# Performance work log

Measured on AMD Instinct MI355X. Metric: run time of the kernel, lower is better.

## Reference

```python
import jax, jax.numpy as jnp
import numpy as np
from jax import lax

N = 128   # batch
H = 1024  # hidden size h
D = 1024  # output size d


def setup_inputs() -> dict:
    key = jax.random.key(0)
    k = jax.random.split(key, 7)
    s_ih = 1.0 / np.sqrt(H)
    inp = {
        "hT": jax.random.normal(k[0], (N, H), dtype=jnp.float32),
        # LSTMCell params (PyTorch layout: [4h, h], gate order i,f,g,o)
        "W_ih": jax.random.uniform(k[1], (4 * H, H), dtype=jnp.float32, minval=-s_ih, maxval=s_ih),
        "W_hh": jax.random.uniform(k[2], (4 * H, H), dtype=jnp.float32, minval=-s_ih, maxval=s_ih),
        "b_ih": jax.random.uniform(k[3], (4 * H,), dtype=jnp.float32, minval=-s_ih, maxval=s_ih),
        "b_hh": jax.random.uniform(k[4], (4 * H,), dtype=jnp.float32, minval=-s_ih, maxval=s_ih),
        # fc1: Linear(h, d)
        "W_fc": jax.random.uniform(k[5], (D, H), dtype=jnp.float32, minval=-s_ih, maxval=s_ih),
        "b_fc": jax.random.uniform(k[6], (D,), dtype=jnp.float32, minval=-s_ih, maxval=s_ih),
        "t": 256,
    }
    return inp


def reference(hT, W_ih, W_hh, b_ih, b_hh, W_fc, b_fc, t):
    n, h = hT.shape

    def step(carry, _):
        x, hx, cx = carry  # x: LSTM input this step; at step 0 it is hT, else prev h
        gates = x @ W_ih.T + b_ih + hx @ W_hh.T + b_hh  # [n, 4h]
        i, f, g, o = jnp.split(gates, 4, axis=-1)
        i = jax.nn.sigmoid(i)
        f = jax.nn.sigmoid(f)
        g = jnp.tanh(g)
        o = jax.nn.sigmoid(o)
        c_new = f * cx + i * g
        h_new = o * jnp.tanh(c_new)
        # next input is the hidden state just produced (all_hs[-1])
        return (h_new, h_new, c_new), h_new

    zeros = jnp.zeros_like(hT)
    _, hs = lax.scan(step, (hT, zeros, zeros), None, length=t)  # [t, n, h]
    recons = hs @ W_fc.T + b_fc  # [t, n, d]
    return jnp.transpose(recons, (1, 0, 2))  # [n, t, d]
```

## Files before the change

### kernel.cpp

```cpp
#include <hip/hip_runtime.h>

#define Hh 1024
#define NBATCH 128
#define TSTEPS 256
#define DOUT 1024
#define SLOT (NBATCH * Hh)

typedef _Float16 half8 __attribute__((ext_vector_type(8)));
typedef float floatx4 __attribute__((ext_vector_type(4)));

__device__ __forceinline__ float fast_sigmoid(float x) {
  float e = __expf(-x);
  return __builtin_amdgcn_rcpf(1.0f + e);
}
__device__ __forceinline__ float fast_tanh(float x) {
  x = fminf(15.0f, fmaxf(-15.0f, x));
  float e = __expf(-2.0f * x);
  return 1.0f - 2.0f * e * __builtin_amdgcn_rcpf(1.0f + e);
}

__global__ void prep_kernel(const float* __restrict__ W_ih, const float* __restrict__ W_hh,
                            const float* __restrict__ W_fc, const float* __restrict__ b_ih,
                            const float* __restrict__ b_hh, const float* __restrict__ hT,
                            _Float16* __restrict__ w_ih_h, _Float16* __restrict__ w_sum_h,
                            _Float16* __restrict__ w_fc_h, float* __restrict__ b_sum,
                            _Float16* __restrict__ hs0, unsigned* __restrict__ flags) {
  int i0 = blockIdx.x * blockDim.x + threadIdx.x;
  int stride = gridDim.x * blockDim.x;
  for (int i = i0; i < 4096 * 1024; i += stride) {
    float a = W_ih[i];
    w_ih_h[i] = (_Float16)a;
    w_sum_h[i] = (_Float16)(a + W_hh[i]);
  }
  for (int i = i0; i < 1024 * 1024; i += stride) w_fc_h[i] = (_Float16)W_fc[i];
  for (int i = i0; i < 4096; i += stride) b_sum[i] = b_ih[i] + b_hh[i];
  for (int i = i0; i < NBATCH * Hh; i += stride) hs0[i] = (_Float16)hT[i];
  for (int i = i0; i < 512; i += stride) flags[i] = 0;
}

__global__ __launch_bounds__(512, 2) void lstm_kernel(
    const _Float16* __restrict__ w_ih_h, const _Float16* __restrict__ w_sum_h,
    const float* __restrict__ b_sum, _Float16* __restrict__ hs,
    unsigned* __restrict__ flags, const _Float16* __restrict__ w_fc,
    const float* __restrict__ b_fc, float* __restrict__ out) {
  unsigned* xcd_ctr = flags + 256;
  const int tid = threadIdx.x;
  const int wave = tid >> 6;
  const int lane = tid & 63;
  const int l15 = lane & 15;
  const int quad = lane >> 4;

  __shared__ unsigned role_sh;
  {
    unsigned xcd;
    asm volatile("s_getreg_b32 %0, hwreg(HW_REG_XCC_ID)" : "=s"(xcd));
    if (tid == 0) role_sh = (xcd << 8) | atomicAdd(&xcd_ctr[xcd], 1u);
  }
  __syncthreads();
  const int g = role_sh >> 8;
  const int jb = role_sh & 255;
  const int n0 = g * 16;
  const int j0 = jb * 32;
  const int kbase = wave * 128;
  const int oc = wave & 1;
  const int rp = (wave >> 1) & 1;
  const int rr = (wave >> 2) & 1;
  unsigned* gflags = flags + g * 32;
  unsigned* pollp = gflags + wave * 4 + (lane & 3);

  __shared__ float2 part[8][2][4][2][64];
  __shared__ floatx4 fcpart[8][2][64];

  float bias[4];
#pragma unroll
  for (int gt = 0; gt < 4; ++gt) bias[gt] = b_sum[gt * 1024 + j0 + oc * 16 + l15];

  const int fc_col = tid & 31;
  const int fc_row = tid >> 5;
  const float bfc = b_fc[j0 + fc_col];
  const int fc_half = fc_col >> 4;
  const int fc_lsrc = (fc_row >> 2) * 16 + (fc_col & 15);
  const int fc_comp = fc_row & 3;

  half8 B[4][2][4];
  half8 Bfc[2][4];
  float cst = 0.0f;

  auto load_B = [&](const _Float16* w) {
#pragma unroll
    for (int gt = 0; gt < 4; ++gt)
#pragma unroll
      for (int ct = 0; ct < 2; ++ct) {
        const _Float16* p =
            w + (size_t)(gt * 1024 + j0 + ct * 16 + l15) * Hh + kbase + quad * 8;
#pragma unroll
        for (int ks = 0; ks < 4; ++ks) B[gt][ct][ks] = *(const half8*)(p + ks * 32);
      }
  };
  {
#pragma unroll
    for (int ct = 0; ct < 2; ++ct) {
      const _Float16* p = w_fc + (size_t)(j0 + ct * 16 + l15) * Hh + kbase + quad * 8;
#pragma unroll
      for (int ks = 0; ks < 4; ++ks) Bfc[ct][ks] = *(const half8*)(p + ks * 32);
    }
  }

  auto poll = [&](int tgt) {
    while (1) {
      unsigned v = __hip_atomic_load(pollp, __ATOMIC_RELAXED, __HIP_MEMORY_SCOPE_AGENT);
      if (__all((int)(v >= (unsigned)tgt))) break;
    }
  };

  auto do_step = [&](const _Float16* hsrc, _Float16* hdst, int s) {
    poll(s);
    floatx4 acc[2][4] = {};
    floatx4 f0 = {}, f1 = {};
    const _Float16* ap = hsrc + (size_t)(n0 + l15) * Hh + kbase + quad * 8;
#pragma unroll
    for (int ks = 0; ks < 4; ++ks) {
      half8 a = *(const half8*)(ap + ks * 32);
#pragma unroll
      for (int ct = 0; ct < 2; ++ct)
#pragma unroll
        for (int gt = 0; gt < 4; ++gt)
          acc[ct][gt] =
              __builtin_amdgcn_mfma_f32_16x16x32_f16(a, B[gt][ct][ks], acc[ct][gt], 0, 0, 0);
      if (s >= 1) {
        f0 = __builtin_amdgcn_mfma_f32_16x16x32_f16(a, Bfc[0][ks], f0, 0, 0, 0);
        f1 = __builtin_amdgcn_mfma_f32_16x16x32_f16(a, Bfc[1][ks], f1, 0, 0, 0);
      }
    }
#pragma unroll
    for (int ct = 0; ct < 2; ++ct)
#pragma unroll
      for (int gt = 0; gt < 4; ++gt) {
        float2 lo, hi;
        lo.x = acc[ct][gt][0]; lo.y = acc[ct][gt][1];
        hi.x = acc[ct][gt][2]; hi.y = acc[ct][gt][3];
        part[wave][ct][gt][0][lane] = lo;
        part[wave][ct][gt][1][lane] = hi;
      }
    if (s >= 1) {
      fcpart[wave][0][lane] = f0;
      fcpart[wave][1][lane] = f1;
    }
    __syncthreads();

    float gv[4];
#pragma unroll
    for (int gt = 0; gt < 4; ++gt) {
      float s2 = bias[gt];
#pragma unroll
      for (int src = 0; src < 8; ++src) {
        float2 p = part[src][oc][gt][rp][lane];
        s2 += rr ? p.y : p.x;
      }
      gv[gt] = s2;
    }
    {
      float ig = fast_sigmoid(gv[0]);
      float fg = fast_sigmoid(gv[1]);
      float gg = fast_tanh(gv[2]);
      float og = fast_sigmoid(gv[3]);
      float c = fg * cst + ig * gg;
      cst = c;
      float h = og * fast_tanh(c);
      int row = n0 + quad * 4 + rp * 2 + rr;
      _Float16 hv = (_Float16)h;
      unsigned short ub;
      __builtin_memcpy(&ub, &hv, 2);
      __hip_atomic_store((unsigned short*)(hdst + (size_t)row * Hh + j0 + oc * 16 + l15),
                         ub, __ATOMIC_RELAXED, __HIP_MEMORY_SCOPE_AGENT);
    }
    if (s >= 1) {
      float fsum = bfc;
#pragma unroll
      for (int src = 0; src < 8; ++src) fsum += fcpart[src][fc_half][fc_lsrc][fc_comp];
      out[((size_t)(n0 + fc_row) * TSTEPS + (s - 1)) * DOUT + j0 + fc_col] = fsum;
    }
    __syncthreads();
    if (tid == 0) {
      __hip_atomic_store(&gflags[jb], (unsigned)(s + 1), __ATOMIC_RELAXED,
                         __HIP_MEMORY_SCOPE_AGENT);
    }
  };

  load_B(w_ih_h);
  do_step(hs, hs + SLOT, 0);
  load_B(w_sum_h);
  for (int s = 1; s < TSTEPS; ++s)
    do_step(hs + (size_t)s * SLOT, hs + (size_t)(s + 1) * SLOT, s);

  {
    unsigned* ep = gflags + (lane & 31);
    while (1) {
      unsigned v = __hip_atomic_load(ep, __ATOMIC_RELAXED, __HIP_MEMORY_SCOPE_AGENT);
      if (__all((int)(v >= (unsigned)TSTEPS))) break;
    }
    asm volatile("" ::: "memory");
    floatx4 f0 = {}, f1 = {};
    const _Float16* ap =
        hs + (size_t)TSTEPS * SLOT + (size_t)(n0 + l15) * Hh + kbase + quad * 8;
#pragma unroll
    for (int ks = 0; ks < 4; ++ks) {
      half8 a = *(const half8*)(ap + ks * 32);
      f0 = __builtin_amdgcn_mfma_f32_16x16x32_f16(a, Bfc[0][ks], f0, 0, 0, 0);
      f1 = __builtin_amdgcn_mfma_f32_16x16x32_f16(a, Bfc[1][ks], f1, 0, 0, 0);
    }
    fcpart[wave][0][lane] = f0;
    fcpart[wave][1][lane] = f1;
    __syncthreads();
    float fsum = bfc;
#pragma unroll
    for (int src = 0; src < 8; ++src) fsum += fcpart[src][fc_half][fc_lsrc][fc_comp];
    out[((size_t)(n0 + fc_row) * TSTEPS + (TSTEPS - 1)) * DOUT + j0 + fc_col] = fsum;
  }
}

extern "C" void kernel_launch(void* const* d_in, const int* in_sizes, int n_in,
                              void* d_out, int out_size, void* d_ws, size_t ws_size,
                              hipStream_t stream) {
  const float* hT   = (const float*)d_in[0];
  const float* W_ih = (const float*)d_in[1];
  const float* W_hh = (const float*)d_in[2];
  const float* b_ih = (const float*)d_in[3];
  const float* b_hh = (const float*)d_in[4];
  const float* W_fc = (const float*)d_in[5];
  const float* b_fc = (const float*)d_in[6];
  float* out = (float*)d_out;

  char* ws = (char*)d_ws;
  unsigned* flags   = (unsigned*)ws;
  float* b_sum      = (float*)(ws + 4096);
  _Float16* w_ih_h  = (_Float16*)(ws + 65536);
  _Float16* w_sum_h = w_ih_h + (size_t)4096 * 1024;
  _Float16* w_fc_h  = w_sum_h + (size_t)4096 * 1024;
  _Float16* hs      = w_fc_h + (size_t)1024 * 1024;

  prep_kernel<<<4096, 256, 0, stream>>>(W_ih, W_hh, W_fc, b_ih, b_hh, hT,
                                        w_ih_h, w_sum_h, w_fc_h, b_sum, hs, flags);
  lstm_kernel<<<256, 512, 0, stream>>>(w_ih_h, w_sum_h, b_sum, hs, flags,
                                       w_fc_h, b_fc, out);
}
```

Baseline: 984.9 us.

## Fuse weight conversion into LSTM kernel and drop separate prep kernel

Removes the prep kernel that converted W_ih, W_ih+W_hh, W_fc and hT to fp16 in workspace. Each persistent block now loads its fp32 weight slices directly, sums and converts them in registers, reads hT straight for step 0, and sums the biases itself. The flags are cleared with a hipMemsetAsync. This avoids a full pass writing and re-reading about 18 MB of fp16 weights and one kernel launch, at the cost of fp32 loads at startup inside the persistent kernel.

```diff
diff --git a/kernel.cpp b/kernel.cpp
--- a/kernel.cpp
+++ b/kernel.cpp
@@ -19,30 +19,18 @@
   return 1.0f - 2.0f * e * __builtin_amdgcn_rcpf(1.0f + e);
 }
 
-__global__ void prep_kernel(const float* __restrict__ W_ih, const float* __restrict__ W_hh,
-                            const float* __restrict__ W_fc, const float* __restrict__ b_ih,
-                            const float* __restrict__ b_hh, const float* __restrict__ hT,
-                            _Float16* __restrict__ w_ih_h, _Float16* __restrict__ w_sum_h,
-                            _Float16* __restrict__ w_fc_h, float* __restrict__ b_sum,
-                            _Float16* __restrict__ hs0, unsigned* __restrict__ flags) {
-  int i0 = blockIdx.x * blockDim.x + threadIdx.x;
-  int stride = gridDim.x * blockDim.x;
-  for (int i = i0; i < 4096 * 1024; i += stride) {
-    float a = W_ih[i];
-    w_ih_h[i] = (_Float16)a;
-    w_sum_h[i] = (_Float16)(a + W_hh[i]);
-  }
-  for (int i = i0; i < 1024 * 1024; i += stride) w_fc_h[i] = (_Float16)W_fc[i];
-  for (int i = i0; i < 4096; i += stride) b_sum[i] = b_ih[i] + b_hh[i];
-  for (int i = i0; i < NBATCH * Hh; i += stride) hs0[i] = (_Float16)hT[i];
-  for (int i = i0; i < 512; i += stride) flags[i] = 0;
+__device__ __forceinline__ half8 cvt8(float4 x, float4 y) {
+  half8 h = {(_Float16)x.x, (_Float16)x.y, (_Float16)x.z, (_Float16)x.w,
+             (_Float16)y.x, (_Float16)y.y, (_Float16)y.z, (_Float16)y.w};
+  return h;
 }
 
 __global__ __launch_bounds__(512, 2) void lstm_kernel(
-    const _Float16* __restrict__ w_ih_h, const _Float16* __restrict__ w_sum_h,
-    const float* __restrict__ b_sum, _Float16* __restrict__ hs,
-    unsigned* __restrict__ flags, const _Float16* __restrict__ w_fc,
-    const float* __restrict__ b_fc, float* __restrict__ out) {
+    const float* __restrict__ W_ih, const float* __restrict__ W_hh,
+    const float* __restrict__ b_ih, const float* __restrict__ b_hh,
+    const float* __restrict__ hT, const float* __restrict__ W_fc,
+    const float* __restrict__ b_fc, _Float16* __restrict__ hs,
+    unsigned* __restrict__ flags, float* __restrict__ out) {
   unsigned* xcd_ctr = flags + 256;
   const int tid = threadIdx.x;
   const int wave = tid >> 6;
@@ -73,7 +61,10 @@
 
   float bias[4];
 #pragma unroll
-  for (int gt = 0; gt < 4; ++gt) bias[gt] = b_sum[gt * 1024 + j0 + oc * 16 + l15];
+  for (int gt = 0; gt < 4; ++gt) {
+    int idx = gt * 1024 + j0 + oc * 16 + l15;
+    bias[gt] = b_ih[idx] + b_hh[idx];
+  }
 
   const int fc_col = tid & 31;
   const int fc_row = tid >> 5;
@@ -86,23 +77,52 @@
   half8 Bfc[2][4];
   float cst = 0.0f;
 
-  auto load_B = [&](const _Float16* w) {
+  auto load_B_ih = [&]() {
 #pragma unroll
     for (int gt = 0; gt < 4; ++gt)
 #pragma unroll
       for (int ct = 0; ct < 2; ++ct) {
-        const _Float16* p =
-            w + (size_t)(gt * 1024 + j0 + ct * 16 + l15) * Hh + kbase + quad * 8;
-#pragma unroll
-        for (int ks = 0; ks < 4; ++ks) B[gt][ct][ks] = *(const half8*)(p + ks * 32);
+        const float* p =
+            W_ih + (size_t)(gt * 1024 + j0 + ct * 16 + l15) * Hh + kbase + quad * 8;
+#pragma unroll
+        for (int ks = 0; ks < 4; ++ks) {
+          float4 x = *(const float4*)(p + ks * 32);
+          float4 y = *(const float4*)(p + ks * 32 + 4);
+          B[gt][ct][ks] = cvt8(x, y);
+        }
+      }
+  };
+  auto load_B_sum = [&]() {
+#pragma unroll
+    for (int gt = 0; gt < 4; ++gt)
+#pragma unroll
+      for (int ct = 0; ct < 2; ++ct) {
+        size_t off = (size_t)(gt * 1024 + j0 + ct * 16 + l15) * Hh + kbase + quad * 8;
+        const float* p1 = W_ih + off;
+        const float* p2 = W_hh + off;
+#pragma unroll
+        for (int ks = 0; ks < 4; ++ks) {
+          float4 x1 = *(const float4*)(p1 + ks * 32);
+          float4 y1 = *(const float4*)(p1 + ks * 32 + 4);
+          float4 x2 = *(const float4*)(p2 + ks * 32);
+          float4 y2 = *(const float4*)(p2 + ks * 32 + 4);
+          float4 xs = {x1.x + x2.x, x1.y + x2.y, x1.z + x2.z, x1.w + x2.w};
+          float4 ys = {y1.x + y2.x, y1.y + y2.y, y1.z + y2.z, y1.w + y2.w};
+          B[gt][ct][ks] = cvt8(xs, ys);
+        }
       }
   };
   {
 #pragma unroll
     for (int ct = 0; ct < 2; ++ct) {
-      const _Float16* p = w_fc + (size_t)(j0 + ct * 16 + l15) * Hh + kbase + quad * 8;
-#pragma unroll
-      for (int ks = 0; ks < 4; ++ks) Bfc[ct][ks] = *(const half8*)(p + ks * 32);
+      const float* p =
+          W_fc + (size_t)(j0 + ct * 16 + l15) * Hh + kbase + quad * 8;
+#pragma unroll
+      for (int ks = 0; ks < 4; ++ks) {
+        float4 x = *(const float4*)(p + ks * 32);
+        float4 y = *(const float4*)(p + ks * 32 + 4);
+        Bfc[ct][ks] = cvt8(x, y);
+      }
     }
   }
 
@@ -113,23 +133,20 @@
     }
   };
 
-  auto do_step = [&](const _Float16* hsrc, _Float16* hdst, int s) {
-    poll(s);
+  auto step_body = [&](const half8* a, _Float16* hdst, int s) {
     floatx4 acc[2][4] = {};
     floatx4 f0 = {}, f1 = {};
-    const _Float16* ap = hsrc + (size_t)(n0 + l15) * Hh + kbase + quad * 8;
 #pragma unroll
     for (int ks = 0; ks < 4; ++ks) {
-      half8 a = *(const half8*)(ap + ks * 32);
 #pragma unroll
       for (int ct = 0; ct < 2; ++ct)
 #pragma unroll
         for (int gt = 0; gt < 4; ++gt)
           acc[ct][gt] =
-              __builtin_amdgcn_mfma_f32_16x16x32_f16(a, B[gt][ct][ks], acc[ct][gt], 0, 0, 0);
+              __builtin_amdgcn_mfma_f32_16x16x32_f16(a[ks], B[gt][ct][ks], acc[ct][gt], 0, 0, 0);
       if (s >= 1) {
-        f0 = __builtin_amdgcn_mfma_f32_16x16x32_f16(a, Bfc[0][ks], f0, 0, 0, 0);
-        f1 = __builtin_amdgcn_mfma_f32_16x16x32_f16(a, Bfc[1][ks], f1, 0, 0, 0);
+        f0 = __builtin_amdgcn_mfma_f32_16x16x32_f16(a[ks], Bfc[0][ks], f0, 0, 0, 0);
+        f1 = __builtin_amdgcn_mfma_f32_16x16x32_f16(a[ks], Bfc[1][ks], f1, 0, 0, 0);
       }
     }
 #pragma unroll
@@ -187,11 +204,29 @@
     }
   };
 
-  load_B(w_ih_h);
-  do_step(hs, hs + SLOT, 0);
-  load_B(w_sum_h);
-  for (int s = 1; s < TSTEPS; ++s)
-    do_step(hs + (size_t)s * SLOT, hs + (size_t)(s + 1) * SLOT, s);
+  load_B_ih();
+  {
+    half8 a[4];
+    const float* ap = hT + (size_t)(n0 + l15) * Hh + kbase + quad * 8;
+#pragma unroll
+    for (int ks = 0; ks < 4; ++ks) {
+      float4 x = *(const float4*)(ap + ks * 32);
+      float4 y = *(const float4*)(ap + ks * 32 + 4);
+      a[ks] = cvt8(x, y);
+    }
+    step_body(a, hs + SLOT, 0);
+  }
+  load_B_sum();
+  for (int s = 1; s < TSTEPS; ++s) {
+    poll(s);
+    asm volatile("" ::: "memory");
+    half8 a[4];
+    const _Float16* hp =
+        hs + (size_t)s * SLOT + (size_t)(n0 + l15) * Hh + kbase + quad * 8;
+#pragma unroll
+    for (int ks = 0; ks < 4; ++ks) a[ks] = *(const half8*)(hp + ks * 32);
+    step_body(a, hs + (size_t)(s + 1) * SLOT, s);
+  }
 
   {
     unsigned* ep = gflags + (lane & 31);
@@ -232,15 +267,10 @@
   float* out = (float*)d_out;
 
   char* ws = (char*)d_ws;
-  unsigned* flags   = (unsigned*)ws;
-  float* b_sum      = (float*)(ws + 4096);
-  _Float16* w_ih_h  = (_Float16*)(ws + 65536);
-  _Float16* w_sum_h = w_ih_h + (size_t)4096 * 1024;
-  _Float16* w_fc_h  = w_sum_h + (size_t)4096 * 1024;
-  _Float16* hs      = w_fc_h + (size_t)1024 * 1024;
-
-  prep_kernel<<<4096, 256, 0, stream>>>(W_ih, W_hh, W_fc, b_ih, b_hh, hT,
-                                        w_ih_h, w_sum_h, w_fc_h, b_sum, hs, flags);
-  lstm_kernel<<<256, 512, 0, stream>>>(w_ih_h, w_sum_h, b_sum, hs, flags,
-                                       w_fc_h, b_fc, out);
-}
+  unsigned* flags = (unsigned*)ws;
+  _Float16* hs    = (_Float16*)(ws + 65536);
+
+  hipMemsetAsync(flags, 0, 4096, stream);
+  lstm_kernel<<<256, 512, 0, stream>>>(W_ih, W_hh, b_ih, b_hh, hT, W_fc, b_fc,
+                                       hs, flags, out);
+}
```

Result: slower. 1.038 ms (+5.4%).
